# Optimization experiments

Hardware: AMD Instinct MI355X
Metric: run time of the kernel (lower is better)

Reference implementation:

```python
import jax, jax.numpy as jnp
import numpy as np

B, V_IN, V_OUT, C_IN, C_OUT, K, NNZ = 16, 1024, 4096, 128, 256, 18, 16384

def setup_inputs() -> dict:
    key = jax.random.key(0)
    ks = jax.random.split(key, 10)
    def lin(k, fan_in, fan_out):
        s = 1.0 / np.sqrt(fan_in)
        return jax.random.normal(k, (fan_in, fan_out), jnp.float32) * s
    return {
        "x": jax.random.normal(ks[0], (B, V_IN, C_IN), jnp.float32),
        "vals": jax.random.uniform(ks[1], (NNZ,), jnp.float32),
        "W1": lin(ks[2], 1 * C_IN, C_OUT),
        "b1": jnp.zeros((C_OUT,), jnp.float32),
        "Wd3": lin(ks[3], (K // 3) * C_IN, C_OUT // 4),
        "bd3": jnp.zeros((C_OUT // 4,), jnp.float32),
        "W2d3": lin(ks[4], (K // 3 * 2) * C_IN, C_OUT // 4),
        "b2d3": jnp.zeros((C_OUT // 4,), jnp.float32),
        "Wf": lin(ks[5], K * C_IN, C_OUT // 2),
        "bf": jnp.zeros((C_OUT // 2,), jnp.float32),
        "rows": jax.random.randint(ks[6], (NNZ,), 0, V_OUT, jnp.int32),
        "cols": jax.random.randint(ks[7], (NNZ,), 0, V_IN, jnp.int32),
        "spiral_idx": jax.random.randint(ks[8], (V_OUT, K), 0, V_OUT, jnp.int32),
    }

def _pool(x, rows, cols, vals, dim_size):
    # sparse upsample: gather cols, scale, scatter-add to rows
    gathered = x[:, cols, :] * vals[None, :, None]  # [B, nnz, C]
    return jnp.zeros((x.shape[0], dim_size, x.shape[2]), x.dtype).at[:, rows, :].add(gathered)

def _spiral_conv(feat, idx, W, b):
    # gather fixed spiral neighborhoods then shared linear layer
    Bz, V, C = feat.shape[0], idx.shape[0], feat.shape[2]
    g = feat[:, idx.reshape(-1), :].reshape(Bz, V, idx.shape[1] * C)  # [B, V, K*C]
    return g @ W + b

def reference(x, vals, W1, b1, Wd3, bd3, W2d3, b2d3, Wf, bf, rows, cols, spiral_idx):
    out = _pool(x, rows, cols, vals, V_OUT)  # [B, V_OUT, C_IN]
    k = spiral_idx.shape[1]
    short_cut = _spiral_conv(out, spiral_idx[:, :1], W1, b1)
    p_d3 = _spiral_conv(out, spiral_idx[:, : k // 3], Wd3, bd3)
    p_2d3 = _spiral_conv(out, spiral_idx[:, : k // 3 * 2], W2d3, b2d3)
    p = _spiral_conv(out, spiral_idx, Wf, bf)
    f = jnp.concatenate((p, p_2d3, p_d3), axis=2)  # [B, V_OUT, C_OUT]
    return jax.nn.relu(short_cut + f)
```

## Files before the change

kernel.cpp:

```cpp
#include <hip/hip_runtime.h>
#include <hip/hip_bf16.h>

#define B_SZ   16
#define V_IN   1024
#define V_OUT  4096
#define C_IN   128
#define C_OUT  256
#define K_NB   18
#define NNZ    16384
#define K_GEMM (K_NB * C_IN)
#define BK     64
#define NKT    (K_GEMM / BK)

typedef __attribute__((ext_vector_type(8))) short bf16x8;
typedef __attribute__((ext_vector_type(4))) float f32x4;

#define GLOAD16(src, dst) __builtin_amdgcn_global_load_lds( \
    (const __attribute__((address_space(1))) unsigned int*)(src), \
    (__attribute__((address_space(3))) unsigned int*)(dst), 16, 0, 0)

__global__ void zero_counts_kernel(int* counts) {
    int i = blockIdx.x * blockDim.x + threadIdx.x;
    if (i < V_OUT) counts[i] = 0;
}

__global__ void hist_kernel(const int* __restrict__ rows, int* counts) {
    int n = blockIdx.x * blockDim.x + threadIdx.x;
    if (n < NNZ) atomicAdd(&counts[rows[n]], 1);
}

__global__ void scan_kernel(const int* __restrict__ counts, int* offsets, int* cursor) {
    __shared__ int s[1024];
    int t = threadIdx.x;
    int base = t * 4;
    int c0 = counts[base], c1 = counts[base + 1], c2 = counts[base + 2], c3 = counts[base + 3];
    int tot = c0 + c1 + c2 + c3;
    s[t] = tot;
    __syncthreads();
    for (int d = 1; d < 1024; d <<= 1) {
        int v = (t >= d) ? s[t - d] : 0;
        __syncthreads();
        s[t] += v;
        __syncthreads();
    }
    int excl = s[t] - tot;
    offsets[base]     = excl;
    offsets[base + 1] = excl + c0;
    offsets[base + 2] = excl + c0 + c1;
    offsets[base + 3] = excl + c0 + c1 + c2;
    cursor[base]     = excl;
    cursor[base + 1] = excl + c0;
    cursor[base + 2] = excl + c0 + c1;
    cursor[base + 3] = excl + c0 + c1 + c2;
    if (t == 1023) offsets[V_OUT] = s[1023];
}

__global__ void fill_kernel(const int* __restrict__ rows, int* cursor, int* perm) {
    int n = blockIdx.x * blockDim.x + threadIdx.x;
    if (n < NNZ) {
        int r = rows[n];
        int pos = atomicAdd(&cursor[r], 1);
        perm[pos] = n;
    }
}

__global__ __launch_bounds__(128) void pool_kernel(
    const float* __restrict__ x, const float* __restrict__ vals,
    const int* __restrict__ cols, const int* __restrict__ offsets,
    const int* __restrict__ perm, __hip_bfloat16* __restrict__ pool) {
    int r = blockIdx.x;
    int c = threadIdx.x;
    int j0 = offsets[r], j1 = offsets[r + 1];
    float acc[B_SZ];
#pragma unroll
    for (int b = 0; b < B_SZ; ++b) acc[b] = 0.f;
    for (int j = j0; j < j1; ++j) {
        int n = perm[j];
        float v = vals[n];
        const float* xp = x + (size_t)cols[n] * C_IN + c;
#pragma unroll
        for (int b = 0; b < B_SZ; ++b) acc[b] += v * xp[(size_t)b * V_IN * C_IN];
    }
#pragma unroll
    for (int b = 0; b < B_SZ; ++b)
        pool[((size_t)b * V_OUT + r) * C_IN + c] = __float2bfloat16(acc[b]);
}

__global__ void wcomb_kernel(const float* __restrict__ W1, const float* __restrict__ Wd3,
                             const float* __restrict__ W2d3, const float* __restrict__ Wf,
                             __hip_bfloat16* __restrict__ wTs) {
    int idx = blockIdx.x * blockDim.x + threadIdx.x;
    if (idx >= NKT * 16384) return;
    int kt = idx >> 14;
    int c  = (idx >> 3) & 2047;
    int e  = idx & 7;
    int nrow  = c >> 3;
    int kslot = (c & 7) << 4;
    int kb = kslot ^ ((nrow & 7) << 4);
    int r  = kt * 64 + (kb >> 1) + e;
    int col = nrow;
    float v;
    if (col < 128)      v = Wf[r * 128 + col];
    else if (col < 192) v = (r < 1536) ? W2d3[r * 64 + (col - 128)] : 0.f;
    else                v = (r < 768)  ? Wd3[r * 64 + (col - 192)]  : 0.f;
    if (r < 128) v += W1[r * 256 + col];
    wTs[idx] = __float2bfloat16(v);
}

__global__ void bias_kernel(const float* __restrict__ b1, const float* __restrict__ bd3,
                            const float* __restrict__ b2d3, const float* __restrict__ bf,
                            float* __restrict__ bias) {
    int c = threadIdx.x;
    float v = b1[c];
    if (c < 128)      v += bf[c];
    else if (c < 192) v += b2d3[c - 128];
    else              v += bd3[c - 192];
    bias[c] = v;
}

__global__ __launch_bounds__(512, 2) void gemm_kernel(
    const __hip_bfloat16* __restrict__ pool,
    const __hip_bfloat16* __restrict__ wTs,
    const float* __restrict__ bias,
    const int* __restrict__ spiral,
    float* __restrict__ out)
{
    __shared__ __align__(16) char smem[149504];
    int* spl = (int*)(smem + 131072);

    const int tid  = threadIdx.x;
    const int lane = tid & 63;
    const int wid  = tid >> 6;
    const int wm   = (wid >> 2) << 7;
    const int wn   = (wid & 3) << 6;

    const int bid = blockIdx.x;
    const int bm  = ((bid & 7) << 5) + (bid >> 3);
    const int b   = bm >> 4;
    const int v0  = (bm & 15) << 8;

    for (int i = tid; i < 256 * K_NB; i += 512) spl[i] = spiral[v0 * K_NB + i];
    __syncthreads();

    const char* poolBytes = (const char*)(pool + (size_t)b * V_OUT * C_IN);
    const char* wTsBytes  = (const char*)wTs;
    const int tg3 = tid >> 3;
    const int sb  = ((tid & 7) << 4) ^ ((tg3 & 7) << 4);

    auto stageA = [&](int kt) {
        const int j   = kt >> 1;
        const int c0b = (kt & 1) << 7;
        char* dst = smem + ((kt & 1) << 15);
#pragma unroll
        for (int ch = 0; ch < 4; ++ch) {
            int sidx = spl[(ch * 64 + tg3) * K_NB + j];
            GLOAD16(poolBytes + ((size_t)sidx << 8) + (c0b + sb),
                    dst + ((ch << 9) + tid) * 16);
        }
    };
    auto stageB = [&](int kt) {
        const char* src = wTsBytes + ((size_t)kt << 15) + tid * 16;
        char* dst = smem + 65536 + ((kt & 1) << 15);
#pragma unroll
        for (int ch = 0; ch < 4; ++ch)
            GLOAD16(src + (ch << 13), dst + (ch << 13) + tid * 16);
    };

    const int l15   = lane & 15;
    const int swm   = (lane & 7) << 4;
    const int klane = (lane >> 4) << 4;
    const int aRow  = (wm + l15) << 7;
    const int bRow  = (wn + l15) << 7;

    f32x4 acc[8][4] = {};

    stageA(0);
    stageB(0);

#pragma unroll 2
    for (int kt = 0; kt < NKT; ++kt) {
        const int s = kt & 1;
        const char* As = smem + (s << 15);
        const char* Bs = smem + 65536 + (s << 15);

        if (kt + 1 < NKT) {
            stageA(kt + 1);
            asm volatile("s_waitcnt vmcnt(4)" ::: "memory");
        } else {
            asm volatile("s_waitcnt vmcnt(0)" ::: "memory");
        }
        __builtin_amdgcn_s_barrier();
        __builtin_amdgcn_sched_barrier(0);

        bf16x8 a[8], b0, b1;
#pragma unroll
        for (int mi = 0; mi < 8; ++mi)
            a[mi] = *(const bf16x8*)(As + aRow + (mi << 11) + ((0 + klane) ^ swm));
        b0 = *(const bf16x8*)(Bs + bRow + (0 << 11) + ((0 + klane) ^ swm));
        b1 = *(const bf16x8*)(Bs + bRow + (1 << 11) + ((0 + klane) ^ swm));
        __builtin_amdgcn_s_setprio(1);
#pragma unroll
        for (int mi = 0; mi < 8; ++mi) {
            acc[mi][0] = __builtin_amdgcn_mfma_f32_16x16x32_bf16(a[mi], b0, acc[mi][0], 0, 0, 0);
            acc[mi][1] = __builtin_amdgcn_mfma_f32_16x16x32_bf16(a[mi], b1, acc[mi][1], 0, 0, 0);
        }
        __builtin_amdgcn_s_setprio(0);
        b0 = *(const bf16x8*)(Bs + bRow + (2 << 11) + ((0 + klane) ^ swm));
        b1 = *(const bf16x8*)(Bs + bRow + (3 << 11) + ((0 + klane) ^ swm));
        __builtin_amdgcn_s_setprio(1);
#pragma unroll
        for (int mi = 0; mi < 8; ++mi) {
            acc[mi][2] = __builtin_amdgcn_mfma_f32_16x16x32_bf16(a[mi], b0, acc[mi][2], 0, 0, 0);
            acc[mi][3] = __builtin_amdgcn_mfma_f32_16x16x32_bf16(a[mi], b1, acc[mi][3], 0, 0, 0);
        }
        __builtin_amdgcn_s_setprio(0);
        if (kt + 1 < NKT) stageB(kt + 1);
#pragma unroll
        for (int mi = 0; mi < 8; ++mi)
            a[mi] = *(const bf16x8*)(As + aRow + (mi << 11) + ((64 + klane) ^ swm));
        b0 = *(const bf16x8*)(Bs + bRow + (0 << 11) + ((64 + klane) ^ swm));
        b1 = *(const bf16x8*)(Bs + bRow + (1 << 11) + ((64 + klane) ^ swm));
        __builtin_amdgcn_s_setprio(1);
#pragma unroll
        for (int mi = 0; mi < 8; ++mi) {
            acc[mi][0] = __builtin_amdgcn_mfma_f32_16x16x32_bf16(a[mi], b0, acc[mi][0], 0, 0, 0);
            acc[mi][1] = __builtin_amdgcn_mfma_f32_16x16x32_bf16(a[mi], b1, acc[mi][1], 0, 0, 0);
        }
        __builtin_amdgcn_s_setprio(0);
        b0 = *(const bf16x8*)(Bs + bRow + (2 << 11) + ((64 + klane) ^ swm));
        b1 = *(const bf16x8*)(Bs + bRow + (3 << 11) + ((64 + klane) ^ swm));
        __builtin_amdgcn_s_setprio(1);
#pragma unroll
        for (int mi = 0; mi < 8; ++mi) {
            acc[mi][2] = __builtin_amdgcn_mfma_f32_16x16x32_bf16(a[mi], b0, acc[mi][2], 0, 0, 0);
            acc[mi][3] = __builtin_amdgcn_mfma_f32_16x16x32_bf16(a[mi], b1, acc[mi][3], 0, 0, 0);
        }
        __builtin_amdgcn_s_setprio(0);
        __builtin_amdgcn_s_barrier();
        __builtin_amdgcn_sched_barrier(0);
    }

#pragma unroll
    for (int ni = 0; ni < 4; ++ni) {
        int col = wn + ni * 16 + l15;
        float bz = bias[col];
#pragma unroll
        for (int mi = 0; mi < 8; ++mi) {
            int row0 = v0 + wm + mi * 16 + ((lane >> 4) << 2);
#pragma unroll
            for (int r4 = 0; r4 < 4; ++r4) {
                float v = acc[mi][ni][r4] + bz;
                out[((size_t)(b * V_OUT + row0 + r4)) * C_OUT + col] = v > 0.f ? v : 0.f;
            }
        }
    }
}

extern "C" void kernel_launch(void* const* d_in, const int* in_sizes, int n_in,
                              void* d_out, int out_size, void* d_ws, size_t ws_size,
                              hipStream_t stream) {
    const float* x     = (const float*)d_in[0];
    const float* vals  = (const float*)d_in[1];
    const float* W1    = (const float*)d_in[2];
    const float* b1    = (const float*)d_in[3];
    const float* Wd3   = (const float*)d_in[4];
    const float* bd3   = (const float*)d_in[5];
    const float* W2d3  = (const float*)d_in[6];
    const float* b2d3  = (const float*)d_in[7];
    const float* Wf    = (const float*)d_in[8];
    const float* bf    = (const float*)d_in[9];
    const int*   rows  = (const int*)d_in[10];
    const int*   cols  = (const int*)d_in[11];
    const int*   spiral= (const int*)d_in[12];
    float* out = (float*)d_out;

    char* ws = (char*)d_ws;
    __hip_bfloat16* pool = (__hip_bfloat16*)ws;
    __hip_bfloat16* wTs  = (__hip_bfloat16*)(ws + 16777216);
    float* bias          = (float*)(ws + 16777216 + 1179648);
    int*   counts        = (int*)(ws + 16777216 + 1179648 + 1024);
    int*   offsets       = counts + V_OUT;
    int*   cursor        = offsets + V_OUT + 4;
    int*   perm          = cursor + V_OUT;

    zero_counts_kernel<<<(V_OUT + 255) / 256, 256, 0, stream>>>(counts);
    hist_kernel<<<NNZ / 256, 256, 0, stream>>>(rows, counts);
    scan_kernel<<<1, 1024, 0, stream>>>(counts, offsets, cursor);
    fill_kernel<<<NNZ / 256, 256, 0, stream>>>(rows, cursor, perm);
    pool_kernel<<<V_OUT, C_IN, 0, stream>>>(x, vals, cols, offsets, perm, pool);
    wcomb_kernel<<<(NKT * 16384 + 255) / 256, 256, 0, stream>>>(W1, Wd3, W2d3, Wf, wTs);
    bias_kernel<<<1, C_OUT, 0, stream>>>(b1, bd3, b2d3, bf, bias);
    gemm_kernel<<<256, 512, 0, stream>>>(pool, wTs, bias, spiral, out);
}
```

Baseline: 112.0 us.

## Prefetch spiral-gathered A tiles two stages ahead and interleave barriers per MFMA phase

```diff
diff --git a/kernel.cpp b/kernel.cpp
--- a/kernel.cpp
+++ b/kernel.cpp
@@ -140,7 +140,8 @@
     const int v0  = (bm & 15) << 8;
 
     for (int i = tid; i < 256 * K_NB; i += 512) spl[i] = spiral[v0 * K_NB + i];
-    __syncthreads();
+    asm volatile("s_waitcnt vmcnt(0) lgkmcnt(0)" ::: "memory");
+    __builtin_amdgcn_s_barrier();
 
     const char* poolBytes = (const char*)(pool + (size_t)b * V_OUT * C_IN);
     const char* wTsBytes  = (const char*)wTs;
@@ -176,28 +177,25 @@
 
     stageA(0);
     stageB(0);
-
-#pragma unroll 2
-    for (int kt = 0; kt < NKT; ++kt) {
-        const int s = kt & 1;
+    stageA(1);
+    asm volatile("s_waitcnt vmcnt(4)" ::: "memory");
+    __builtin_amdgcn_s_barrier();
+
+    for (int T = 0; T < NKT; ++T) {
+        const int s = T & 1;
         const char* As = smem + (s << 15);
         const char* Bs = smem + 65536 + (s << 15);
-
-        if (kt + 1 < NKT) {
-            stageA(kt + 1);
-            asm volatile("s_waitcnt vmcnt(4)" ::: "memory");
-        } else {
-            asm volatile("s_waitcnt vmcnt(0)" ::: "memory");
-        }
-        __builtin_amdgcn_s_barrier();
-        __builtin_amdgcn_sched_barrier(0);
-
-        bf16x8 a[8], b0, b1;
+        bf16x8 a[8], b0, b1, b2, b3;
+
+        if (T + 1 < NKT) stageB(T + 1);
 #pragma unroll
         for (int mi = 0; mi < 8; ++mi)
             a[mi] = *(const bf16x8*)(As + aRow + (mi << 11) + ((0 + klane) ^ swm));
         b0 = *(const bf16x8*)(Bs + bRow + (0 << 11) + ((0 + klane) ^ swm));
         b1 = *(const bf16x8*)(Bs + bRow + (1 << 11) + ((0 + klane) ^ swm));
+        __builtin_amdgcn_s_barrier();
+        asm volatile("s_waitcnt lgkmcnt(0)" ::: "memory");
+        __builtin_amdgcn_sched_barrier(0);
         __builtin_amdgcn_s_setprio(1);
 #pragma unroll
         for (int mi = 0; mi < 8; ++mi) {
@@ -205,21 +203,28 @@
             acc[mi][1] = __builtin_amdgcn_mfma_f32_16x16x32_bf16(a[mi], b1, acc[mi][1], 0, 0, 0);
         }
         __builtin_amdgcn_s_setprio(0);
-        b0 = *(const bf16x8*)(Bs + bRow + (2 << 11) + ((0 + klane) ^ swm));
-        b1 = *(const bf16x8*)(Bs + bRow + (3 << 11) + ((0 + klane) ^ swm));
+
+        b2 = *(const bf16x8*)(Bs + bRow + (2 << 11) + ((0 + klane) ^ swm));
+        b3 = *(const bf16x8*)(Bs + bRow + (3 << 11) + ((0 + klane) ^ swm));
+        __builtin_amdgcn_s_barrier();
+        asm volatile("s_waitcnt lgkmcnt(0)" ::: "memory");
+        __builtin_amdgcn_sched_barrier(0);
         __builtin_amdgcn_s_setprio(1);
 #pragma unroll
         for (int mi = 0; mi < 8; ++mi) {
-            acc[mi][2] = __builtin_amdgcn_mfma_f32_16x16x32_bf16(a[mi], b0, acc[mi][2], 0, 0, 0);
-            acc[mi][3] = __builtin_amdgcn_mfma_f32_16x16x32_bf16(a[mi], b1, acc[mi][3], 0, 0, 0);
+            acc[mi][2] = __builtin_amdgcn_mfma_f32_16x16x32_bf16(a[mi], b2, acc[mi][2], 0, 0, 0);
+            acc[mi][3] = __builtin_amdgcn_mfma_f32_16x16x32_bf16(a[mi], b3, acc[mi][3], 0, 0, 0);
         }
         __builtin_amdgcn_s_setprio(0);
-        if (kt + 1 < NKT) stageB(kt + 1);
+
 #pragma unroll
         for (int mi = 0; mi < 8; ++mi)
             a[mi] = *(const bf16x8*)(As + aRow + (mi << 11) + ((64 + klane) ^ swm));
         b0 = *(const bf16x8*)(Bs + bRow + (0 << 11) + ((64 + klane) ^ swm));
         b1 = *(const bf16x8*)(Bs + bRow + (1 << 11) + ((64 + klane) ^ swm));
+        __builtin_amdgcn_s_barrier();
+        asm volatile("s_waitcnt lgkmcnt(0)" ::: "memory");
+        __builtin_amdgcn_sched_barrier(0);
         __builtin_amdgcn_s_setprio(1);
 #pragma unroll
         for (int mi = 0; mi < 8; ++mi) {
@@ -227,13 +232,25 @@
             acc[mi][1] = __builtin_amdgcn_mfma_f32_16x16x32_bf16(a[mi], b1, acc[mi][1], 0, 0, 0);
         }
         __builtin_amdgcn_s_setprio(0);
-        b0 = *(const bf16x8*)(Bs + bRow + (2 << 11) + ((64 + klane) ^ swm));
-        b1 = *(const bf16x8*)(Bs + bRow + (3 << 11) + ((64 + klane) ^ swm));
+        __builtin_amdgcn_s_barrier();
+        __builtin_amdgcn_sched_barrier(0);
+
+        b2 = *(const bf16x8*)(Bs + bRow + (2 << 11) + ((64 + klane) ^ swm));
+        b3 = *(const bf16x8*)(Bs + bRow + (3 << 11) + ((64 + klane) ^ swm));
+        if (T + 2 < NKT) {
+            stageA(T + 2);
+            asm volatile("s_waitcnt vmcnt(4)" ::: "memory");
+        } else {
+            asm volatile("s_waitcnt vmcnt(0)" ::: "memory");
+        }
+        __builtin_amdgcn_s_barrier();
+        asm volatile("s_waitcnt lgkmcnt(0)" ::: "memory");
+        __builtin_amdgcn_sched_barrier(0);
         __builtin_amdgcn_s_setprio(1);
 #pragma unroll
         for (int mi = 0; mi < 8; ++mi) {
-            acc[mi][2] = __builtin_amdgcn_mfma_f32_16x16x32_bf16(a[mi], b0, acc[mi][2], 0, 0, 0);
-            acc[mi][3] = __builtin_amdgcn_mfma_f32_16x16x32_bf16(a[mi], b1, acc[mi][3], 0, 0, 0);
+            acc[mi][2] = __builtin_amdgcn_mfma_f32_16x16x32_bf16(a[mi], b2, acc[mi][2], 0, 0, 0);
+            acc[mi][3] = __builtin_amdgcn_mfma_f32_16x16x32_bf16(a[mi], b3, acc[mi][3], 0, 0, 0);
         }
         __builtin_amdgcn_s_setprio(0);
         __builtin_amdgcn_s_barrier();
```

Result: slower. 115.0 us (+2.7%).
